# Performance work log

Hardware: AMD Instinct MI355X
Metric: run time of the kernel (lower is better)

Reference implementation:

```python
import jax, jax.numpy as jnp
import numpy as np

ALPHA = 16.0
R = 8.0
SCALE = ALPHA / R  # scaling = alpha / r, same for every adapter


def setup_inputs() -> dict:
    key = jax.random.key(0)
    ks = jax.random.split(key, 5)
    B_, S, D = 4, 2048, 4096
    E, r = 8, 8
    x = jax.random.normal(ks[0], (B_, S, D), dtype=jnp.float32)
    W = jax.random.normal(ks[1], (D, D), dtype=jnp.float32) * (1.0 / np.sqrt(D))
    b = jax.random.normal(ks[2], (D,), dtype=jnp.float32) * 0.02
    A = jax.random.normal(ks[3], (E, r, D), dtype=jnp.float32) * (1.0 / np.sqrt(D))
    Bm = jax.random.normal(ks[4], (E, D, r), dtype=jnp.float32) * 0.02
    return {"x": x, "W": W, "b": b, "A": A, "B": Bm}


def reference(x, W, b, A, B):
    # base = F.linear(x, W, b)
    base = jnp.einsum('bsi,oi->bso', x, W) + b
    # lora_total = sum_e scale * (x @ A_e.T @ B_e.T); all experts stacked.
    # intermediate [B,S,E,r] is tiny (r=8)
    t = jnp.einsum('bsi,eri->bser', x, A)
    lora = jnp.einsum('bser,eor->bso', t, B) * SCALE
    return base + lora
```

## Files before the change

kernel.cpp:

```cpp
#include <hip/hip_runtime.h>
#include <hip/hip_bf16.h>

typedef unsigned short u16;
typedef __bf16 bf16x8 __attribute__((ext_vector_type(8)));
typedef float f32x4 __attribute__((ext_vector_type(4)));

constexpr int Mdim = 8192;
constexpr int Ndim = 4096;
constexpr int Kdim = 4096;
constexpr int ER   = 64;
constexpr float LSCALE = 2.0f;

__device__ __forceinline__ u16 f2bf(float f) {
    union { float f; unsigned u; } v; v.f = f;
    unsigned r = v.u + 0x7fffu + ((v.u >> 16) & 1u);
    return (u16)(r >> 16);
}

#define GLOAD_LDS16(g, l)                                             \
    __builtin_amdgcn_global_load_lds(                                 \
        (const __attribute__((address_space(1))) void*)(g),           \
        (__attribute__((address_space(3))) void*)(l), 16, 0, 0)

__global__ __launch_bounds__(256) void fused_pre_kernel(
    const float* __restrict__ x, const float* __restrict__ W,
    const float* __restrict__ A, const float* __restrict__ Bm,
    u16* __restrict__ Xb, u16* __restrict__ Wb)
{
    __shared__ __align__(16) float sAc[ER][128];
    __shared__ __align__(16) float sBc[64][ER];

    const int bx = blockIdx.x;
    const int t  = threadIdx.x;

    if ((bx % 9) != 8) {
        const int ci = (bx / 9) * 8 + (bx % 9);
        const size_t i = ((size_t)ci * 256 + t) * 8;
        const float4 v0 = *(const float4*)(x + i);
        const float4 v1 = *(const float4*)(x + i + 4);
        uint4 o;
        o.x = (unsigned)f2bf(v0.x) | ((unsigned)f2bf(v0.y) << 16);
        o.y = (unsigned)f2bf(v0.z) | ((unsigned)f2bf(v0.w) << 16);
        o.z = (unsigned)f2bf(v1.x) | ((unsigned)f2bf(v1.y) << 16);
        o.w = (unsigned)f2bf(v1.z) | ((unsigned)f2bf(v1.w) << 16);
        *(uint4*)(Xb + i) = o;
        return;
    }

    const int w  = bx / 9;
    const int i0 = (w & 31) * 128;
    const int o0 = (w >> 5) * 64;

#pragma unroll
    for (int p = 0; p < 8; ++p) {
        int lin = p * 1024 + t * 4;
        int er = lin >> 7, ci2 = lin & 127;
        *(float4*)&sAc[er][ci2] = *(const float4*)(A + (size_t)er * Kdim + i0 + ci2);
    }
    {
        int ol = t >> 2;
        int c  = (t & 3) * 16;
#pragma unroll
        for (int q = 0; q < 2; ++q) {
            int er = c + q * 8;
            int e  = er >> 3;
            const float* src = Bm + ((size_t)e * Ndim + (o0 + ol)) * 8;
            *(float4*)&sBc[ol][er]     = *(const float4*)(src);
            *(float4*)&sBc[ol][er + 4] = *(const float4*)(src + 4);
        }
    }
    __syncthreads();

    const int tx = t & 31;
    const int ty = t >> 5;
    float acc[8][4] = {};
#pragma unroll 4
    for (int er = 0; er < ER; ++er) {
        float4 a = *(const float4*)&sAc[er][tx * 4];
#pragma unroll
        for (int q = 0; q < 8; ++q) {
            float bv = sBc[q * 8 + ty][er];
            acc[q][0] += bv * a.x;
            acc[q][1] += bv * a.y;
            acc[q][2] += bv * a.z;
            acc[q][3] += bv * a.w;
        }
    }
#pragma unroll
    for (int q = 0; q < 8; ++q) {
        int o = o0 + q * 8 + ty;
        const float4 wv4 = *(const float4*)(W + (size_t)o * Kdim + i0 + tx * 4);
        ushort4 st;
        st.x = f2bf(wv4.x + LSCALE * acc[q][0]);
        st.y = f2bf(wv4.y + LSCALE * acc[q][1]);
        st.z = f2bf(wv4.z + LSCALE * acc[q][2]);
        st.w = f2bf(wv4.w + LSCALE * acc[q][3]);
        *(ushort4*)(Wb + (size_t)o * Kdim + i0 + tx * 4) = st;
    }
}

constexpr int BM = 256, BN = 256, BK = 64;

__global__ __launch_bounds__(512, 2) void gemm_bias_kernel(
    const u16* __restrict__ Xb, const u16* __restrict__ Wb,
    const float* __restrict__ bias, float* __restrict__ C)
{
    __shared__ __align__(16) u16 lds[65536];

    const int t    = threadIdx.x;
    const int lane = t & 63;
    const int wv   = t >> 6;
    const int wr   = wv >> 2;
    const int wc   = wv & 3;

    const int wg  = blockIdx.x;
    const int xcd = wg & 7, lid = wg >> 3;
    const int mt  = (xcd & 1) * 16 + (lid >> 2);
    const int ntl = (xcd >> 1) * 4 + (lid & 3);
    const int bm  = mt * BM;
    const int bn  = ntl * BN;

    u16* buf0 = lds;
    u16* buf1 = lds + 32768;

    const int rl  = t >> 3;
    const int scl = ((t ^ (t >> 3)) & 7) * 8;
    const u16* aSrc0 = Xb + (size_t)(bm + rl) * Kdim + scl;
    const u16* aSrc1 = Xb + (size_t)(bm + 128 + rl) * Kdim + scl;
    const u16* bSrc0 = Wb + (size_t)(bn + rl) * Kdim + scl;
    const u16* bSrc1 = Wb + (size_t)(bn + 128 + rl) * Kdim + scl;
    constexpr size_t R64 = (size_t)64 * Kdim;

#define STG(BUF, SLOT, SRCP, KO)                                              \
    do {                                                                      \
        GLOAD_LDS16((SRCP) + (KO), (BUF) + (SLOT) + t * 8);                   \
        GLOAD_LDS16((SRCP) + (KO) + R64, (BUF) + (SLOT) + 4096 + t * 8);      \
    } while (0)

    const int fr  = lane & 15;
    const int cp0 = (((lane >> 4) ^ (lane & 7)) & 7) * 8;
    const int cp1 = ((((lane >> 4) + 4) ^ (lane & 7)) & 7) * 8;
    const int aB  = wr * 8192;
    const int bB  = 16384 + (wc >> 1) * 8192 + (wc & 1) * 4096;

    f32x4 acc[8][4];
#pragma unroll
    for (int i = 0; i < 8; ++i)
#pragma unroll
        for (int j = 0; j < 4; ++j)
            acc[i][j] = f32x4{0.f, 0.f, 0.f, 0.f};

    bf16x8 af[4][2];
    bf16x8 bf0[2][2];
    bf16x8 bf1[2][2];

#define DS_A(BUF, MH)                                                         \
    _Pragma("unroll")                                                         \
    for (int mi = 0; mi < 4; ++mi) {                                          \
        const int rb = aB + ((MH) * 64 + mi * 16 + fr) * 64;                  \
        af[mi][0] = *(const bf16x8*)&(BUF)[rb + cp0];                         \
        af[mi][1] = *(const bf16x8*)&(BUF)[rb + cp1];                         \
    }

#define DS_B(BUF, NH, BF)                                                     \
    _Pragma("unroll")                                                         \
    for (int ni = 0; ni < 2; ++ni) {                                          \
        const int rb = bB + ((NH) * 32 + ni * 16 + fr) * 64;                  \
        BF[ni][0] = *(const bf16x8*)&(BUF)[rb + cp0];                         \
        BF[ni][1] = *(const bf16x8*)&(BUF)[rb + cp1];                         \
    }

#define MQ(MH, NH, BF)                                                        \
    __builtin_amdgcn_s_setprio(1);                                            \
    _Pragma("unroll")                                                         \
    for (int mi = 0; mi < 4; ++mi)                                            \
        _Pragma("unroll")                                                     \
        for (int ni = 0; ni < 2; ++ni) {                                      \
            acc[(MH)*4 + mi][(NH)*2 + ni] =                                   \
                __builtin_amdgcn_mfma_f32_16x16x32_bf16(                      \
                    af[mi][0], BF[ni][0], acc[(MH)*4 + mi][(NH)*2 + ni],      \
                    0, 0, 0);                                                 \
            acc[(MH)*4 + mi][(NH)*2 + ni] =                                   \
                __builtin_amdgcn_mfma_f32_16x16x32_bf16(                      \
                    af[mi][1], BF[ni][1], acc[(MH)*4 + mi][(NH)*2 + ni],      \
                    0, 0, 0);                                                 \
        }                                                                     \
    __builtin_amdgcn_s_setprio(0);

#define FENCE asm volatile("" ::: "memory")
#define BAR   __builtin_amdgcn_s_barrier(); FENCE
#define LGKM0 asm volatile("s_waitcnt lgkmcnt(0)" ::: "memory");              \
              __builtin_amdgcn_sched_barrier(0)
#define VM6   asm volatile("s_waitcnt vmcnt(6)" ::: "memory")
#define LGK8  asm volatile("s_waitcnt lgkmcnt(8)" ::: "memory")

    STG(buf0, 16384, bSrc0, 0);
    STG(buf0, 24576, bSrc1, 0);
    STG(buf0, 0,     aSrc0, 0);
    STG(buf0, 8192,  aSrc1, 0);
    STG(buf1, 16384, bSrc0, 64);
    STG(buf1, 24576, bSrc1, 64);
    STG(buf1, 0,     aSrc0, 64);
    VM6;
    BAR;

#pragma unroll 1
    for (int g = 0; g < 32; ++g) {
        const int koO  = (2 * g + 1) * 64;
        const int koE2 = ((2 * g + 2) & 63) * 64;
        const int koO2 = ((2 * g + 3) & 63) * 64;

        DS_A(buf0, 0); DS_B(buf0, 0, bf0);
        STG(buf1, 8192, aSrc1, koO);
        LGK8;
        BAR; LGKM0; MQ(0, 0, bf0); BAR;
        DS_B(buf0, 1, bf1);
        STG(buf0, 16384, bSrc0, koE2);
        BAR; LGKM0; MQ(0, 1, bf1); BAR;
        DS_A(buf0, 1);
        STG(buf0, 24576, bSrc1, koE2);
        BAR; LGKM0; MQ(1, 1, bf1); BAR;
        STG(buf0, 0, aSrc0, koE2);
        VM6;
        BAR; MQ(1, 0, bf0); BAR;
        DS_A(buf1, 0); DS_B(buf1, 0, bf0);
        STG(buf0, 8192, aSrc1, koE2);
        LGK8;
        BAR; LGKM0; MQ(0, 0, bf0); BAR;
        DS_B(buf1, 1, bf1);
        STG(buf1, 16384, bSrc0, koO2);
        BAR; LGKM0; MQ(0, 1, bf1); BAR;
        DS_A(buf1, 1);
        STG(buf1, 24576, bSrc1, koO2);
        BAR; LGKM0; MQ(1, 1, bf1); BAR;
        STG(buf1, 0, aSrc0, koO2);
        VM6;
        BAR; MQ(1, 0, bf0); BAR;
    }

#undef STG
#undef DS_A
#undef DS_B
#undef MQ

#pragma unroll
    for (int ni = 0; ni < 4; ++ni) {
        const int col = bn + wc * 64 + ni * 16 + (lane & 15);
        const float bv = bias[col];
#pragma unroll
        for (int mi = 0; mi < 8; ++mi) {
            const int rbase = bm + wr * 128 + mi * 16 + (lane >> 4) * 4;
#pragma unroll
            for (int j = 0; j < 4; ++j)
                C[(size_t)(rbase + j) * Ndim + col] = acc[mi][ni][j] + bv;
        }
    }
}

__global__ __launch_bounds__(256) void naive_row_kernel(
    const float* __restrict__ x, const float* __restrict__ W,
    const float* __restrict__ bias, const float* __restrict__ A,
    const float* __restrict__ Bm, float* __restrict__ out)
{
    __shared__ float sx[Kdim];
    __shared__ float st[ER];
    const int m = blockIdx.x;
    const float* xr = x + (size_t)m * Kdim;
    for (int i = threadIdx.x; i < Kdim; i += 256) sx[i] = xr[i];
    __syncthreads();
    if (threadIdx.x < ER) {
        const float* ar = A + (size_t)threadIdx.x * Kdim;
        float s = 0.f;
        for (int i = 0; i < Kdim; ++i) s += sx[i] * ar[i];
        st[threadIdx.x] = s;
    }
    __syncthreads();
    for (int o = threadIdx.x; o < Ndim; o += 256) {
        const float* wr = W + (size_t)o * Kdim;
        float s = bias[o];
        for (int i = 0; i < Kdim; ++i) s += sx[i] * wr[i];
        float l = 0.f;
        for (int e = 0; e < 8; ++e) {
            const float* bp = Bm + ((size_t)e * Ndim + o) * 8;
            for (int r = 0; r < 8; ++r) l += st[e * 8 + r] * bp[r];
        }
        out[(size_t)m * Ndim + o] = s + LSCALE * l;
    }
}

extern "C" void kernel_launch(void* const* d_in, const int* in_sizes, int n_in,
                              void* d_out, int out_size, void* d_ws, size_t ws_size,
                              hipStream_t stream)
{
    const float* x  = (const float*)d_in[0];
    const float* W  = (const float*)d_in[1];
    const float* b  = (const float*)d_in[2];
    const float* A  = (const float*)d_in[3];
    const float* Bm = (const float*)d_in[4];
    float* out = (float*)d_out;

    const size_t xb_bytes = (size_t)Mdim * Kdim * 2;
    const size_t wb_bytes = (size_t)Ndim * Kdim * 2;

    if (ws_size >= xb_bytes + wb_bytes) {
        u16* Xb = (u16*)d_ws;
        u16* Wb = (u16*)((char*)d_ws + xb_bytes);
        fused_pre_kernel<<<18432, 256, 0, stream>>>(x, W, A, Bm, Xb, Wb);
        gemm_bias_kernel<<<dim3((Mdim / BM) * (Ndim / BN)), 512, 0, stream>>>(Xb, Wb, b, out);
    } else {
        naive_row_kernel<<<Mdim, 256, 0, stream>>>(x, W, b, A, Bm, out);
    }
}
```

Measured before the change: 290.6 us.

## Software-pipeline LDS fragment loads so each MFMA quarter overlaps the next load

Restructures the main GEMM loop so every MFMA quarter runs while the next fragment set is being read from LDS. All four B fragments per k-step are loaded at once and two A register sets are kept live. The last quarter of each step is deferred into the next phase, with a trailing call after the loop. The goal is to hide LDS read latency behind matrix-core work, at the cost of more VGPRs (extra A and B fragment buffers) and a more complex schedule.

```diff
diff --git a/kernel.cpp b/kernel.cpp
--- a/kernel.cpp
+++ b/kernel.cpp
@@ -151,26 +151,27 @@
             acc[i][j] = f32x4{0.f, 0.f, 0.f, 0.f};
 
     bf16x8 af[4][2];
-    bf16x8 bf0[2][2];
-    bf16x8 bf1[2][2];
-
-#define DS_A(BUF, MH)                                                         \
+    bf16x8 ah[4][2];
+    bf16x8 bP[4][2];
+    bf16x8 bQ[4][2];
+
+#define DS_A(BUF, MH, AR)                                                     \
     _Pragma("unroll")                                                         \
     for (int mi = 0; mi < 4; ++mi) {                                          \
         const int rb = aB + ((MH) * 64 + mi * 16 + fr) * 64;                  \
-        af[mi][0] = *(const bf16x8*)&(BUF)[rb + cp0];                         \
-        af[mi][1] = *(const bf16x8*)&(BUF)[rb + cp1];                         \
-    }
-
-#define DS_B(BUF, NH, BF)                                                     \
+        AR[mi][0] = *(const bf16x8*)&(BUF)[rb + cp0];                         \
+        AR[mi][1] = *(const bf16x8*)&(BUF)[rb + cp1];                         \
+    }
+
+#define DS_B(BUF, BR)                                                         \
     _Pragma("unroll")                                                         \
-    for (int ni = 0; ni < 2; ++ni) {                                          \
-        const int rb = bB + ((NH) * 32 + ni * 16 + fr) * 64;                  \
-        BF[ni][0] = *(const bf16x8*)&(BUF)[rb + cp0];                         \
-        BF[ni][1] = *(const bf16x8*)&(BUF)[rb + cp1];                         \
-    }
-
-#define MQ(MH, NH, BF)                                                        \
+    for (int ni = 0; ni < 4; ++ni) {                                          \
+        const int rb = bB + (ni * 16 + fr) * 64;                              \
+        BR[ni][0] = *(const bf16x8*)&(BUF)[rb + cp0];                         \
+        BR[ni][1] = *(const bf16x8*)&(BUF)[rb + cp1];                         \
+    }
+
+#define MQ(AR, BR, MH, NH)                                                    \
     __builtin_amdgcn_s_setprio(1);                                            \
     _Pragma("unroll")                                                         \
     for (int mi = 0; mi < 4; ++mi)                                            \
@@ -178,12 +179,12 @@
         for (int ni = 0; ni < 2; ++ni) {                                      \
             acc[(MH)*4 + mi][(NH)*2 + ni] =                                   \
                 __builtin_amdgcn_mfma_f32_16x16x32_bf16(                      \
-                    af[mi][0], BF[ni][0], acc[(MH)*4 + mi][(NH)*2 + ni],      \
-                    0, 0, 0);                                                 \
+                    AR[mi][0], BR[(NH)*2 + ni][0],                            \
+                    acc[(MH)*4 + mi][(NH)*2 + ni], 0, 0, 0);                  \
             acc[(MH)*4 + mi][(NH)*2 + ni] =                                   \
                 __builtin_amdgcn_mfma_f32_16x16x32_bf16(                      \
-                    af[mi][1], BF[ni][1], acc[(MH)*4 + mi][(NH)*2 + ni],      \
-                    0, 0, 0);                                                 \
+                    AR[mi][1], BR[(NH)*2 + ni][1],                            \
+                    acc[(MH)*4 + mi][(NH)*2 + ni], 0, 0, 0);                  \
         }                                                                     \
     __builtin_amdgcn_s_setprio(0);
 
@@ -192,7 +193,6 @@
 #define LGKM0 asm volatile("s_waitcnt lgkmcnt(0)" ::: "memory");              \
               __builtin_amdgcn_sched_barrier(0)
 #define VM6   asm volatile("s_waitcnt vmcnt(6)" ::: "memory")
-#define LGK8  asm volatile("s_waitcnt lgkmcnt(8)" ::: "memory")
 
     STG(buf0, 16384, bSrc0, 0);
     STG(buf0, 24576, bSrc1, 0);
@@ -210,33 +210,35 @@
         const int koE2 = ((2 * g + 2) & 63) * 64;
         const int koO2 = ((2 * g + 3) & 63) * 64;
 
-        DS_A(buf0, 0); DS_B(buf0, 0, bf0);
+        DS_B(buf0, bP);
         STG(buf1, 8192, aSrc1, koO);
-        LGK8;
-        BAR; LGKM0; MQ(0, 0, bf0); BAR;
-        DS_B(buf0, 1, bf1);
+        BAR; LGKM0;
+        if (g != 0) { MQ(ah, bQ, 1, 0); }
+        BAR;
+        DS_A(buf0, 0, af);
         STG(buf0, 16384, bSrc0, koE2);
-        BAR; LGKM0; MQ(0, 1, bf1); BAR;
-        DS_A(buf0, 1);
+        BAR; LGKM0; MQ(af, bP, 0, 0); BAR;
+        DS_A(buf0, 1, ah);
         STG(buf0, 24576, bSrc1, koE2);
-        BAR; LGKM0; MQ(1, 1, bf1); BAR;
+        BAR; LGKM0; MQ(af, bP, 0, 1); BAR;
         STG(buf0, 0, aSrc0, koE2);
         VM6;
-        BAR; MQ(1, 0, bf0); BAR;
-        DS_A(buf1, 0); DS_B(buf1, 0, bf0);
+        BAR; MQ(ah, bP, 1, 1); BAR;
+
+        DS_B(buf1, bQ);
         STG(buf0, 8192, aSrc1, koE2);
-        LGK8;
-        BAR; LGKM0; MQ(0, 0, bf0); BAR;
-        DS_B(buf1, 1, bf1);
+        BAR; LGKM0; MQ(ah, bP, 1, 0); BAR;
+        DS_A(buf1, 0, af);
         STG(buf1, 16384, bSrc0, koO2);
-        BAR; LGKM0; MQ(0, 1, bf1); BAR;
-        DS_A(buf1, 1);
+        BAR; LGKM0; MQ(af, bQ, 0, 0); BAR;
+        DS_A(buf1, 1, ah);
         STG(buf1, 24576, bSrc1, koO2);
-        BAR; LGKM0; MQ(1, 1, bf1); BAR;
+        BAR; LGKM0; MQ(af, bQ, 0, 1); BAR;
         STG(buf1, 0, aSrc0, koO2);
         VM6;
-        BAR; MQ(1, 0, bf0); BAR;
-    }
+        BAR; MQ(ah, bQ, 1, 1); BAR;
+    }
+    MQ(ah, bQ, 1, 0);
 
 #undef STG
 #undef DS_A
```

Result: slower. 296.7 us (+2.1%).
